# Performance work log

Hardware: AMD Instinct MI355X
Metric: run time of the kernel (lower is better)

Reference implementation:

```python
import jax, jax.numpy as jnp
import numpy as np

NUM_CLASSES = 40
EOS_COEF = 0.1
IGNORE = 255
W_CLASS, W_MASK, W_DICE = 2.0, 5.0, 5.0
EPS = 1e-8


def setup_inputs() -> dict:
    key = jax.random.key(0)
    k1, k2, k3, k4 = jax.random.split(key, 4)
    B, Q, H, W = 4, 100, 256, 256
    pred_logits = jax.random.normal(k1, (B, Q, NUM_CLASSES + 1), dtype=jnp.float32)
    pred_masks = jax.random.normal(k2, (B, Q, H, W), dtype=jnp.float32)
    targets = jax.random.randint(k3, (B, H, W), 0, NUM_CLASSES)
    ign = jax.random.uniform(k4, (B, H, W)) < 0.05
    targets = jnp.where(ign, IGNORE, targets).astype(jnp.int32)
    return {"pred_logits": pred_logits, "pred_masks": pred_masks, "targets": targets}


def reference(pred_logits, pred_masks, targets):
    B, Q, _ = pred_logits.shape
    C = NUM_CLASSES
    f32 = jnp.float32
    valid = targets != IGNORE                      # [B,H,W]
    tgt_safe = jnp.where(valid, targets, 0)        # in-range for indexing

    # ---- loss_labels: pixel->query assignment, per-query mode label ----
    # sigmoid is monotone, so argmax over queries of raw logits == argmax of sigmoid
    assign = jnp.argmax(pred_masks, axis=1)        # [B,H,W]
    b_idx = jnp.broadcast_to(jnp.arange(B)[:, None, None], targets.shape)
    # counts[b,q,c] = #valid pixels assigned to query q with label c
    counts = jnp.zeros((B, Q, C), f32).at[b_idx, assign, tgt_safe].add(valid.astype(f32))
    has_pix = counts.sum(-1) > 0                   # [B,Q]
    # mode = argmax of counts (ties -> smallest class, matching torch.mode)
    target_classes = jnp.where(has_pix, jnp.argmax(counts, axis=-1), C)  # [B,Q]

    logp = jax.nn.log_softmax(pred_logits, axis=-1)                      # [B,Q,C+1]
    nll = -jnp.take_along_axis(logp, target_classes[..., None], axis=-1)[..., 0]
    empty_weight = jnp.ones(C + 1, f32).at[-1].set(EOS_COEF)
    # ignore_index = num_classes in the CE over classes
    ce = jnp.where(target_classes != C, nll * empty_weight[target_classes], 0.0)
    p = jnp.exp(-ce)
    loss_ce = jnp.mean((1.0 - p) ** 2 * ce)

    # ---- loss_masks: per-pixel CE over queries + per-class dice ----
    logp_pix = jax.nn.log_softmax(pred_masks, axis=1)                    # [B,Q,H,W]
    nll_pix = -jnp.take_along_axis(logp_pix, tgt_safe[:, None], axis=1)[:, 0]  # [B,H,W]
    n_valid = valid.astype(f32).sum()
    ce_mask = jnp.sum(jnp.where(valid, nll_pix, 0.0)) / jnp.maximum(n_valid, 1.0)

    sig = jax.nn.sigmoid(pred_masks)                                     # [B,Q,H,W]
    tmask = (targets[:, None] == jnp.arange(C)[None, :, None, None]).astype(f32)  # [B,C,H,W]
    vm = valid[:, None].astype(f32)                                      # [B,1,H,W]
    inter = jnp.einsum('bqhw,bchw->bqc', sig, tmask * vm)                # numerator uses valid mask
    src_sum = sig.sum(axis=(2, 3))                                       # [B,Q]
    tsum = tmask.sum(axis=(2, 3))                                        # [B,C]
    dice = 2.0 * inter / (src_sum[:, :, None] + tsum[:, None, :] + EPS)  # [B,Q,C]
    present = tsum.sum(axis=0) > 0                                       # [C]
    dice_loss = jnp.sum(jnp.where(present, 1.0 - dice.mean(axis=(0, 1)), 0.0)) / C

    combined = W_MASK * ce_mask + W_DICE * dice_loss
    return W_CLASS * loss_ce + combined
```

## Files before the change

kernel.cpp:

```cpp
#include <hip/hip_runtime.h>
#include <hip/hip_bf16.h>

constexpr int B = 4, Q = 100, C = 40, Cp1 = 41, HW = 65536;
constexpr int NPIX = B * HW;

constexpr int QT = 7;
constexpr int ROWS = B * QT;
constexpr int SEGS = 128;
constexpr int KSEG = HW / SEGS;
constexpr int BWAVES = ROWS * SEGS;
constexpr int BBLK = BWAVES / 4;

constexpr int ATHR = 256, APX = 2;
constexpr int ABLKS = NPIX / (ATHR * APX);
constexpr int ASLOT = HW / (ATHR * APX);
constexpr int QU = 5;

constexpr int GRID = BBLK + ABLKS;

constexpr int WS_WORDS = 32562;

typedef __attribute__((ext_vector_type(8))) short short8;
typedef __attribute__((ext_vector_type(4))) float f32x4;

__device__ __forceinline__ short f2bf(float f) {
    unsigned u = __float_as_uint(f);
    u += 0x7FFF + ((u >> 16) & 1);
    return (short)(u >> 16);
}

__global__ void kZ(unsigned* __restrict__ ws, int n) {
    int i = blockIdx.x * blockDim.x + threadIdx.x;
    for (; i < n; i += gridDim.x * blockDim.x) ws[i] = 0u;
}

__global__ __launch_bounds__(256) void kBig(const float* __restrict__ masks,
                                            const int* __restrict__ targets,
                                            unsigned* __restrict__ counts,
                                            unsigned* __restrict__ tsum,
                                            float* __restrict__ ce_sum,
                                            unsigned* __restrict__ n_valid,
                                            float* __restrict__ inter_ext) {
    __shared__ float smem[4 * C];
    int tid = threadIdx.x;
    int blk = blockIdx.x;
    int lane = tid & 63, wave = tid >> 6;

    int grp = blk / 11, rem = blk - grp * 11;
    bool isA = rem < 4;

    if (!isA) {
        int bblk = grp * 7 + (rem - 4);
        int w = bblk * 4 + wave;
        int row = w >> 7;
        int seg = w & (SEGS - 1);
        int b = row / QT, qt = row - b * QT;
        int q0 = qt * 16;
        int k0 = seg * KSEG;
        int m = lane & 15, quad = lane >> 4;
        int qa = q0 + m; if (qa > 99) qa = 0;
        const float* ap = masks + ((size_t)b * Q + qa) * HW + k0 + quad * 8;
        const int*   tp = targets + (size_t)b * HW + k0 + quad * 8;
        int cv0 = m, cv1 = 16 + m;
        int cv2 = (m == 8) ? 255 : 32 + m;

        f32x4 acc0 = {0.f, 0.f, 0.f, 0.f};
        f32x4 acc1 = {0.f, 0.f, 0.f, 0.f};
        f32x4 acc2 = {0.f, 0.f, 0.f, 0.f};

        #pragma unroll 2
        for (int step = 0; step < KSEG / 32; ++step) {
            int k = step * 32;
            float4 x0 = *(const float4*)(ap + k);
            float4 x1 = *(const float4*)(ap + k + 4);
            int4 t0 = *(const int4*)(tp + k);
            int4 t1 = *(const int4*)(tp + k + 4);
            float xs[8] = {x0.x, x0.y, x0.z, x0.w, x1.x, x1.y, x1.z, x1.w};
            int tss[8] = {t0.x, t0.y, t0.z, t0.w, t1.x, t1.y, t1.z, t1.w};
            short8 av, b0, b1, b2;
            #pragma unroll
            for (int j = 0; j < 8; ++j) {
                float sg = __builtin_amdgcn_rcpf(1.f + __expf(-xs[j]));
                av[j] = f2bf(sg);
                b0[j] = (tss[j] == cv0) ? (short)0x3F80 : (short)0;
                b1[j] = (tss[j] == cv1) ? (short)0x3F80 : (short)0;
                b2[j] = (tss[j] == cv2) ? (short)0x3F80 : (short)0;
            }
            acc0 = __builtin_amdgcn_mfma_f32_16x16x32_bf16(av, b0, acc0, 0, 0, 0);
            acc1 = __builtin_amdgcn_mfma_f32_16x16x32_bf16(av, b1, acc1, 0, 0, 0);
            acc2 = __builtin_amdgcn_mfma_f32_16x16x32_bf16(av, b2, acc2, 0, 0, 0);
        }

        #pragma unroll
        for (int reg = 0; reg < 4; ++reg) {
            int q = q0 + quad * 4 + reg;
            if (q < 100) {
                size_t base = (size_t)(b * Q + q) * Cp1;
                atomicAdd(&inter_ext[base + m], acc0[reg]);
                atomicAdd(&inter_ext[base + 16 + m], acc1[reg]);
                if (m <= 8) atomicAdd(&inter_ext[base + 32 + m], acc2[reg]);
            }
        }
    } else {
        unsigned* ts_local = (unsigned*)&smem[0];
        float*    cred     = &smem[64];
        unsigned* vred     = (unsigned*)&smem[72];

        int ablk = grp * 4 + rem;
        int b = ablk / ASLOT;
        int hw = (ablk % ASLOT) * (ATHR * APX) + tid * APX;
        const float* mp = masks + (size_t)b * Q * HW + hw;
        int2 tg = *(const int2*)(targets + (size_t)b * HW + hw);
        int tgs[2] = {tg.x, tg.y};

        float m2[2] = {-INFINITY, -INFINITY}, s[2] = {0.f, 0.f}, xt[2] = {0.f, 0.f};
        int amax[2] = {0, 0};

        for (int qq = 0; qq < Q; qq += QU) {
            float2 vv[QU];
            #pragma unroll
            for (int u = 0; u < QU; ++u)
                vv[u] = *(const float2*)(mp + (size_t)(qq + u) * HW);
            #pragma unroll
            for (int u = 0; u < QU; ++u) {
                int q = qq + u;
                float v[2] = {vv[u].x, vv[u].y};
                #pragma unroll
                for (int j = 0; j < 2; ++j) {
                    s[j] += __expf(v[j]);
                    amax[j] = (v[j] > m2[j]) ? q : amax[j];
                    m2[j] = fmaxf(m2[j], v[j]);
                    xt[j] = (q == tgs[j]) ? v[j] : xt[j];
                }
            }
        }

        if (tid < C) ts_local[tid] = 0u;
        __syncthreads();

        float ce = 0.f;
        unsigned nv = 0;
        #pragma unroll
        for (int j = 0; j < 2; ++j) {
            if (tgs[j] != 255) {
                ce += __logf(s[j]) - xt[j];
                nv++;
                atomicAdd(&counts[((size_t)b * Q + amax[j]) * C + tgs[j]], 1u);
                atomicAdd(&ts_local[tgs[j]], 1u);
            }
        }
        for (int off = 32; off; off >>= 1) {
            ce += __shfl_xor(ce, off);
            nv += __shfl_xor(nv, off);
        }
        if (lane == 0) { cred[wave] = ce; vred[wave] = nv; }
        __syncthreads();
        if (tid == 0) {
            atomicAdd(ce_sum, cred[0] + cred[1] + cred[2] + cred[3]);
            atomicAdd(n_valid, vred[0] + vred[1] + vred[2] + vred[3]);
        }
        if (tid < C) {
            unsigned t = ts_local[tid];
            if (t) atomicAdd(&tsum[b * C + tid], t);
        }
    }
}

__global__ __launch_bounds__(512) void kC(const float* __restrict__ logits,
                                          const unsigned* __restrict__ counts,
                                          const unsigned* __restrict__ tsum,
                                          const float* __restrict__ inter_ext,
                                          const float* __restrict__ ce_sum,
                                          const unsigned* __restrict__ n_valid,
                                          float* __restrict__ out) {
    int tid = threadIdx.x;
    __shared__ float dice_sum[C];
    __shared__ float ssum[B * Q];
    __shared__ float wred[8];
    __shared__ float s_lce;
    if (tid < C) dice_sum[tid] = 0.f;
    if (tid < B * Q) {
        const float* r = inter_ext + (size_t)tid * Cp1;
        float t = 0.f;
        #pragma unroll
        for (int c = 0; c < Cp1; ++c) t += r[c];
        ssum[tid] = t;
    }

    float ce_acc = 0.f;
    for (int i = tid; i < B * Q; i += 512) {
        const unsigned* cnt = counts + (size_t)i * C;
        unsigned best = 0;
        int tc = C;
        #pragma unroll
        for (int c = 0; c < C; ++c) {
            unsigned v = cnt[c];
            if (v > best) { best = v; tc = c; }
        }
        if (tc != C) {
            const float* lg = logits + (size_t)i * Cp1;
            float mm = -INFINITY, xt = 0.f;
            #pragma unroll
            for (int c = 0; c < Cp1; ++c) {
                float v = lg[c];
                mm = fmaxf(mm, v);
                if (c == tc) xt = v;
            }
            float ss = 0.f;
            #pragma unroll
            for (int c = 0; c < Cp1; ++c) ss += __expf(lg[c] - mm);
            float nll = mm + __logf(ss) - xt;
            float p = __expf(-nll);
            float om = 1.f - p;
            ce_acc += om * om * nll;
        }
    }
    for (int off = 32; off; off >>= 1) ce_acc += __shfl_xor(ce_acc, off);
    if ((tid & 63) == 0) wred[tid >> 6] = ce_acc;
    __syncthreads();
    if (tid == 0) {
        float t = 0.f;
        for (int w = 0; w < 8; ++w) t += wred[w];
        s_lce = t;
    }

    for (int i = tid; i < B * Q * C; i += 512) {
        int bq = i / C, c = i - bq * C;
        float denom = ssum[bq] + (float)tsum[(bq / Q) * C + c] + 1e-8f;
        atomicAdd(&dice_sum[c], 2.f * inter_ext[(size_t)bq * Cp1 + c] / denom);
    }
    __syncthreads();

    if (tid == 0) {
        float dl = 0.f;
        for (int c = 0; c < C; ++c) {
            unsigned ts = tsum[c] + tsum[C + c] + tsum[2 * C + c] + tsum[3 * C + c];
            if (ts > 0) dl += 1.f - dice_sum[c] * (1.f / (B * Q));
        }
        dl *= (1.f / C);
        float ce_mask = ce_sum[0] / fmaxf((float)n_valid[0], 1.f);
        float lce = s_lce * (1.f / (B * Q));
        out[0] = 2.f * lce + 5.f * ce_mask + 5.f * dl;
    }
}

extern "C" void kernel_launch(void* const* d_in, const int* in_sizes, int n_in,
                              void* d_out, int out_size, void* d_ws, size_t ws_size,
                              hipStream_t stream) {
    const float* logits  = (const float*)d_in[0];
    const float* masks   = (const float*)d_in[1];
    const int*   targets = (const int*)d_in[2];
    float* out = (float*)d_out;

    unsigned* ws        = (unsigned*)d_ws;
    unsigned* counts    = ws;
    unsigned* tsum      = ws + 16000;
    float*    ce_sum    = (float*)(ws + 16160);
    unsigned* n_valid   = ws + 16161;
    float*    inter_ext = (float*)(ws + 16162);

    kZ<<<64, 256, 0, stream>>>(ws, WS_WORDS);
    kBig<<<GRID, 256, 0, stream>>>(masks, targets, counts, tsum, ce_sum, n_valid,
                                   inter_ext);
    kC<<<1, 512, 0, stream>>>(logits, counts, tsum, inter_ext, ce_sum, n_valid, out);
}
```

Before: 221.4 us.

## Fuse per-pixel CE pass and dice MFMA pass into one read of masks

Previously the big kernel split its blocks into two roles that each read the full 105MB mask tensor: one did softmax/argmax per pixel, the other did sigmoid plus MFMA for the dice intersection. The new kernel reads each mask tile once. It computes the CE/argmax statistics and the bf16 sigmoids together, stages the sigmoids in a swizzled LDS tile with byte-packed targets, and runs the MFMA intersection from LDS in three of the four waves. This halves global memory traffic but adds two barriers per 16-query tile, leaves one wave idle during the MFMA phase, and issues more atomics per tile.

```diff
diff --git a/kernel.cpp b/kernel.cpp
--- a/kernel.cpp
+++ b/kernel.cpp
@@ -1,22 +1,8 @@
 #include <hip/hip_runtime.h>
-#include <hip/hip_bf16.h>
 
 constexpr int B = 4, Q = 100, C = 40, Cp1 = 41, HW = 65536;
-constexpr int NPIX = B * HW;
-
-constexpr int QT = 7;
-constexpr int ROWS = B * QT;
-constexpr int SEGS = 128;
-constexpr int KSEG = HW / SEGS;
-constexpr int BWAVES = ROWS * SEGS;
-constexpr int BBLK = BWAVES / 4;
-
-constexpr int ATHR = 256, APX = 2;
-constexpr int ABLKS = NPIX / (ATHR * APX);
-constexpr int ASLOT = HW / (ATHR * APX);
-constexpr int QU = 5;
-
-constexpr int GRID = BBLK + ABLKS;
+
+constexpr int FBLKS = 512;
 
 constexpr int WS_WORDS = 32562;
 
@@ -34,135 +20,137 @@
     for (; i < n; i += gridDim.x * blockDim.x) ws[i] = 0u;
 }
 
-__global__ __launch_bounds__(256) void kBig(const float* __restrict__ masks,
-                                            const int* __restrict__ targets,
-                                            unsigned* __restrict__ counts,
-                                            unsigned* __restrict__ tsum,
-                                            float* __restrict__ ce_sum,
-                                            unsigned* __restrict__ n_valid,
-                                            float* __restrict__ inter_ext) {
-    __shared__ float smem[4 * C];
-    int tid = threadIdx.x;
-    int blk = blockIdx.x;
-    int lane = tid & 63, wave = tid >> 6;
-
-    int grp = blk / 11, rem = blk - grp * 11;
-    bool isA = rem < 4;
-
-    if (!isA) {
-        int bblk = grp * 7 + (rem - 4);
-        int w = bblk * 4 + wave;
-        int row = w >> 7;
-        int seg = w & (SEGS - 1);
-        int b = row / QT, qt = row - b * QT;
-        int q0 = qt * 16;
-        int k0 = seg * KSEG;
-        int m = lane & 15, quad = lane >> 4;
-        int qa = q0 + m; if (qa > 99) qa = 0;
-        const float* ap = masks + ((size_t)b * Q + qa) * HW + k0 + quad * 8;
-        const int*   tp = targets + (size_t)b * HW + k0 + quad * 8;
-        int cv0 = m, cv1 = 16 + m;
-        int cv2 = (m == 8) ? 255 : 32 + m;
-
-        f32x4 acc0 = {0.f, 0.f, 0.f, 0.f};
-        f32x4 acc1 = {0.f, 0.f, 0.f, 0.f};
-        f32x4 acc2 = {0.f, 0.f, 0.f, 0.f};
-
-        #pragma unroll 2
-        for (int step = 0; step < KSEG / 32; ++step) {
-            int k = step * 32;
-            float4 x0 = *(const float4*)(ap + k);
-            float4 x1 = *(const float4*)(ap + k + 4);
-            int4 t0 = *(const int4*)(tp + k);
-            int4 t1 = *(const int4*)(tp + k + 4);
-            float xs[8] = {x0.x, x0.y, x0.z, x0.w, x1.x, x1.y, x1.z, x1.w};
-            int tss[8] = {t0.x, t0.y, t0.z, t0.w, t1.x, t1.y, t1.z, t1.w};
-            short8 av, b0, b1, b2;
-            #pragma unroll
-            for (int j = 0; j < 8; ++j) {
-                float sg = __builtin_amdgcn_rcpf(1.f + __expf(-xs[j]));
-                av[j] = f2bf(sg);
-                b0[j] = (tss[j] == cv0) ? (short)0x3F80 : (short)0;
-                b1[j] = (tss[j] == cv1) ? (short)0x3F80 : (short)0;
-                b2[j] = (tss[j] == cv2) ? (short)0x3F80 : (short)0;
-            }
-            acc0 = __builtin_amdgcn_mfma_f32_16x16x32_bf16(av, b0, acc0, 0, 0, 0);
-            acc1 = __builtin_amdgcn_mfma_f32_16x16x32_bf16(av, b1, acc1, 0, 0, 0);
-            acc2 = __builtin_amdgcn_mfma_f32_16x16x32_bf16(av, b2, acc2, 0, 0, 0);
-        }
-
-        #pragma unroll
-        for (int reg = 0; reg < 4; ++reg) {
-            int q = q0 + quad * 4 + reg;
-            if (q < 100) {
-                size_t base = (size_t)(b * Q + q) * Cp1;
-                atomicAdd(&inter_ext[base + m], acc0[reg]);
-                atomicAdd(&inter_ext[base + 16 + m], acc1[reg]);
-                if (m <= 8) atomicAdd(&inter_ext[base + 32 + m], acc2[reg]);
-            }
-        }
-    } else {
-        unsigned* ts_local = (unsigned*)&smem[0];
-        float*    cred     = &smem[64];
-        unsigned* vred     = (unsigned*)&smem[72];
-
-        int ablk = grp * 4 + rem;
-        int b = ablk / ASLOT;
-        int hw = (ablk % ASLOT) * (ATHR * APX) + tid * APX;
-        const float* mp = masks + (size_t)b * Q * HW + hw;
-        int2 tg = *(const int2*)(targets + (size_t)b * HW + hw);
-        int tgs[2] = {tg.x, tg.y};
-
-        float m2[2] = {-INFINITY, -INFINITY}, s[2] = {0.f, 0.f}, xt[2] = {0.f, 0.f};
-        int amax[2] = {0, 0};
-
-        for (int qq = 0; qq < Q; qq += QU) {
-            float2 vv[QU];
-            #pragma unroll
-            for (int u = 0; u < QU; ++u)
-                vv[u] = *(const float2*)(mp + (size_t)(qq + u) * HW);
-            #pragma unroll
-            for (int u = 0; u < QU; ++u) {
-                int q = qq + u;
-                float v[2] = {vv[u].x, vv[u].y};
+__global__ __launch_bounds__(256) void kF(const float* __restrict__ masks,
+                                          const int* __restrict__ targets,
+                                          unsigned* __restrict__ counts,
+                                          unsigned* __restrict__ tsum,
+                                          float* __restrict__ ce_sum,
+                                          unsigned* __restrict__ n_valid,
+                                          float* __restrict__ inter_ext) {
+    __shared__ __align__(16) short tileS[16 * 512];
+    __shared__ __align__(8) unsigned char tgt8[512];
+    __shared__ float smem[160];
+
+    const int tid = threadIdx.x;
+    const int l = tid & 63, w = tid >> 6;
+    const int m = l & 15, quad = l >> 4;
+
+    const int blk = blockIdx.x;
+    const int b = blk >> 7;
+    const int seg = blk & 127;
+    const int pxb = w * 128 + 2 * l;
+    const int p0 = seg * 512 + pxb;
+
+    const int2 tg = *(const int2*)(targets + (size_t)b * HW + p0);
+    *(unsigned short*)&tgt8[pxb] =
+        (unsigned short)((tg.x & 255) | ((tg.y & 255) << 8));
+    unsigned* ts_local = (unsigned*)&smem[0];
+    if (tid < C) ts_local[tid] = 0u;
+    __syncthreads();
+
+    const float* mp = masks + (size_t)b * Q * HW + p0;
+    const int tg0 = tg.x, tg1 = tg.y;
+
+    float m20 = -INFINITY, m21 = -INFINITY;
+    float s0 = 0.f, s1 = 0.f, xt0 = 0.f, xt1 = 0.f;
+    int am0 = 0, am1 = 0;
+
+    char* tbytes = (char*)tileS;
+    const int wbase = w * 256 + l * 4;
+
+    const int colbase = w * 16;
+    const int cv = (w == 2) ? ((m == 8) ? 255 : 32 + m) : (colbase + m);
+
+    for (int qt = 0; qt < 7; ++qt) {
+        const int nu = (qt == 6) ? 4 : 16;
+
+        float2 vv[16];
+        const float* mq = mp + (size_t)(qt * 16) * HW;
+        #pragma unroll
+        for (int u = 0; u < 16; ++u)
+            if (u < nu) vv[u] = *(const float2*)(mq + (size_t)u * HW);
+
+        #pragma unroll
+        for (int u = 0; u < 16; ++u)
+            if (u < nu) {
+                const int q = qt * 16 + u;
+                const float v0 = vv[u].x, v1 = vv[u].y;
+                s0 += __expf(v0);
+                s1 += __expf(v1);
+                am0 = (v0 > m20) ? q : am0;  m20 = fmaxf(m20, v0);
+                am1 = (v1 > m21) ? q : am1;  m21 = fmaxf(m21, v1);
+                xt0 = (q == tg0) ? v0 : xt0;
+                xt1 = (q == tg1) ? v1 : xt1;
+                const float g0 = __builtin_amdgcn_rcpf(1.f + __expf(-v0));
+                const float g1 = __builtin_amdgcn_rcpf(1.f + __expf(-v1));
+                const unsigned pk = (unsigned)(unsigned short)f2bf(g0) |
+                                    ((unsigned)(unsigned short)f2bf(g1) << 16);
+                *(unsigned*)(tbytes + ((u * 1024 + wbase) ^ ((u & 7) << 4))) = pk;
+            }
+
+        asm volatile("s_waitcnt lgkmcnt(0)" ::: "memory");
+        __builtin_amdgcn_s_barrier();
+        asm volatile("" ::: "memory");
+
+        f32x4 acc = {0.f, 0.f, 0.f, 0.f};
+        if (w < 3) {
+            #pragma unroll
+            for (int kc = 0; kc < 16; ++kc) {
+                const short8 av = *(const short8*)(tbytes +
+                    ((m * 1024 + kc * 64 + quad * 16) ^ ((m & 7) << 4)));
+                const unsigned long long tw =
+                    *(const unsigned long long*)&tgt8[kc * 32 + quad * 8];
+                short8 bv;
                 #pragma unroll
-                for (int j = 0; j < 2; ++j) {
-                    s[j] += __expf(v[j]);
-                    amax[j] = (v[j] > m2[j]) ? q : amax[j];
-                    m2[j] = fmaxf(m2[j], v[j]);
-                    xt[j] = (q == tgs[j]) ? v[j] : xt[j];
+                for (int j = 0; j < 8; ++j) {
+                    const int tb = (int)((tw >> (8 * j)) & 255);
+                    bv[j] = (tb == cv) ? (short)0x3F80 : (short)0;
                 }
-            }
-        }
-
-        if (tid < C) ts_local[tid] = 0u;
-        __syncthreads();
-
-        float ce = 0.f;
-        unsigned nv = 0;
-        #pragma unroll
-        for (int j = 0; j < 2; ++j) {
-            if (tgs[j] != 255) {
-                ce += __logf(s[j]) - xt[j];
-                nv++;
-                atomicAdd(&counts[((size_t)b * Q + amax[j]) * C + tgs[j]], 1u);
-                atomicAdd(&ts_local[tgs[j]], 1u);
-            }
-        }
-        for (int off = 32; off; off >>= 1) {
-            ce += __shfl_xor(ce, off);
-            nv += __shfl_xor(nv, off);
-        }
-        if (lane == 0) { cred[wave] = ce; vred[wave] = nv; }
-        __syncthreads();
-        if (tid == 0) {
-            atomicAdd(ce_sum, cred[0] + cred[1] + cred[2] + cred[3]);
-            atomicAdd(n_valid, vred[0] + vred[1] + vred[2] + vred[3]);
-        }
-        if (tid < C) {
-            unsigned t = ts_local[tid];
-            if (t) atomicAdd(&tsum[b * C + tid], t);
-        }
+                acc = __builtin_amdgcn_mfma_f32_16x16x32_bf16(av, bv, acc, 0, 0, 0);
+            }
+        }
+        asm volatile("" ::: "memory");
+        __builtin_amdgcn_s_barrier();
+        asm volatile("" ::: "memory");
+
+        if (w < 3 && !(w == 2 && m > 8)) {
+            #pragma unroll
+            for (int reg = 0; reg < 4; ++reg) {
+                const int q = qt * 16 + quad * 4 + reg;
+                if (q < 100)
+                    atomicAdd(&inter_ext[(size_t)(b * Q + q) * Cp1 + colbase + m],
+                              acc[reg]);
+            }
+        }
+    }
+
+    float ce = 0.f;
+    unsigned nv = 0u;
+    if (tg0 != 255) {
+        ce += __logf(s0) - xt0; nv++;
+        atomicAdd(&counts[((size_t)b * Q + am0) * C + tg0], 1u);
+        atomicAdd(&ts_local[tg0], 1u);
+    }
+    if (tg1 != 255) {
+        ce += __logf(s1) - xt1; nv++;
+        atomicAdd(&counts[((size_t)b * Q + am1) * C + tg1], 1u);
+        atomicAdd(&ts_local[tg1], 1u);
+    }
+    for (int off = 32; off; off >>= 1) {
+        ce += __shfl_xor(ce, off);
+        nv += __shfl_xor(nv, off);
+    }
+    float* cred = &smem[64];
+    unsigned* vred = (unsigned*)&smem[72];
+    if (l == 0) { cred[w] = ce; vred[w] = nv; }
+    __syncthreads();
+    if (tid == 0) {
+        atomicAdd(ce_sum, cred[0] + cred[1] + cred[2] + cred[3]);
+        atomicAdd(n_valid, vred[0] + vred[1] + vred[2] + vred[3]);
+    }
+    if (tid < C) {
+        unsigned t = ts_local[tid];
+        if (t) atomicAdd(&tsum[b * C + tid], t);
     }
 }
 
@@ -260,7 +248,7 @@
     float*    inter_ext = (float*)(ws + 16162);
 
     kZ<<<64, 256, 0, stream>>>(ws, WS_WORDS);
-    kBig<<<GRID, 256, 0, stream>>>(masks, targets, counts, tsum, ce_sum, n_valid,
-                                   inter_ext);
+    kF<<<FBLKS, 256, 0, stream>>>(masks, targets, counts, tsum, ce_sum, n_valid,
+                                  inter_ext);
     kC<<<1, 512, 0, stream>>>(logits, counts, tsum, inter_ext, ce_sum, n_valid, out);
 }
```

Result: no change. 220.7 us (-0.3%).
